# Performance work log

Measured on AMD Instinct MI355X. Metric: run time of the kernel, lower is better.

The kernel has to match this reference:

```python
import jax, jax.numpy as jnp
import numpy as np
import math

# Module constants (from __init__ defaults / chosen init_kwargs)
B = 4            # hand_batch_size
C = 8            # num_cameras
BC = B * C       # camera batch
R = 256          # resolution
NB = 64          # num_bins
BIN = 0.0136     # bin_size
FOV = 33.0       # degrees
DCS = 0.001      # camera_sensor_distance
SIGMA_BIN = 3.0  # self.sigma for soft binning


def _masks():
    fov_rad = FOV * math.pi / 180.0
    scale = math.tan(fov_rad / 2.0)
    center_scale = scale * (1.0 - 1.0 / R)
    lin = jnp.linspace(-center_scale, center_scale, R, dtype=jnp.float32)
    xg, yg = jnp.meshgrid(lin, lin, indexing='xy')
    fm = jnp.stack([xg, -yg, -jnp.ones((R, R), jnp.float32)], axis=2)
    film_mask = -fm / jnp.linalg.norm(fm, axis=2, keepdims=True)  # [R,R,3]
    cos_mask = 1.0 / jnp.sqrt(xg * xg + yg * yg + 1.0)            # [R,R]
    return film_mask, cos_mask


def setup_inputs() -> dict:
    key = jax.random.key(0)
    k1, k2 = jax.random.split(key)
    film_mask, cos_mask = _masks()
    # per-pixel interpolated vertex normals (pre-normalization, as dr.interpolate output)
    normals = jax.random.normal(k1, (BC, R, R, 3), dtype=jnp.float32)
    # per-pixel camera-space intersection points; z ~ 0.5 m so depths fall mid-histogram
    intersections = jax.random.normal(k2, (BC, R, R, 3), dtype=jnp.float32) * 0.1 \
        + jnp.array([0.0, 0.0, 0.5], dtype=jnp.float32)
    return {"normals": normals, "intersections": intersections,
            "film_mask": film_mask, "cos_mask": cos_mask}


def reference(normals, intersections, film_mask, cos_mask):
    width = 2.0 * math.tan(FOV * math.pi / 360.0)
    # cosine foreshortening w.r.t. film ray directions
    dots = jnp.clip(jnp.einsum('ijk,bijk->bij', film_mask, normals), 0.0, 1.0)
    # laser origin offset by 2 * camera_sensor_distance along +x
    laser_points = intersections - jnp.array([2.0 * DCS, 0.0, 0.0], dtype=intersections.dtype)
    laser_distances = jnp.linalg.norm(laser_points, axis=3)  # [BC,R,R]
    laser_tan = jnp.sqrt(laser_points[..., 0] ** 2 + laser_points[..., 1] ** 2) / laser_points[..., 2]
    sig = math.tan(math.radians(21.5)) / 1.4
    laser_mask = jnp.exp(-laser_tan ** 2 / (2.0 * sig * sig))
    dots = dots * laser_mask
    radiance = dots / laser_distances / laser_distances / math.pi \
        * (width * width) * (cos_mask ** 3) / float(R * R)      # [BC,R,R]
    depths = (jnp.linalg.norm(intersections, axis=3) + laser_distances) / 2.0
    d_bin = depths / BIN                                         # [BC,R,R]
    b = jnp.arange(NB, dtype=jnp.float32)                        # [NB]
    # soft bin kernel: sigmoid(s*(d-b)) - sigmoid(s*(d-b-1)), [BC,R,R,NB]
    x = d_bin[..., None] - b
    kernels = jax.nn.sigmoid(SIGMA_BIN * x) - jax.nn.sigmoid(SIGMA_BIN * (x - 1.0))
    # histogram accumulation over all pixels -> per-camera transient [BC,NB]
    transients = jnp.einsum('bijk,bij->bk', kernels, radiance)
    return transients
```

## Files before the change

### kernel.cpp

```cpp
#include <hip/hip_runtime.h>
#include <math.h>

#define NPIX    65536
#define NBINS   64
#define NBATCH  32
#define SPLIT   32
#define BLOCKT  256
#define PXPT    4
#define ITERS   (NPIX / SPLIT / (BLOCKT * PXPT))
#define WIN     12
#define HSTRIDE 68
#define NG      (BLOCKT / 2)
#define SCRATCH (4 * NBINS)
#define LDSN    (NG * HSTRIDE + SCRATCH)

#define THREE_LOG2E 4.328085122666891f

static __device__ __forceinline__ void rmw12(float* hp, const float* W) {
    float4* h4 = (float4*)hp;
    float4 a = h4[0], bb = h4[1], c = h4[2];
    a.x  += W[0];  a.y  += W[1];  a.z  += W[2];  a.w  += W[3];
    bb.x += W[4];  bb.y += W[5];  bb.z += W[6];  bb.w += W[7];
    c.x  += W[8];  c.y  += W[9];  c.z  += W[10]; c.w  += W[11];
    h4[0] = a; h4[1] = bb; h4[2] = c;
}

__global__ __launch_bounds__(BLOCKT, 4) void spad_hist_kernel(
    const float* __restrict__ normals,
    const float* __restrict__ inters,
    const float* __restrict__ film,
    const float* __restrict__ cosm,
    float* __restrict__ ws,
    float kconst, float lmask_c, float half_inv_bin,
    float xstep, float xneg)
{
    __shared__ float hist[LDSN];
    const int tid = threadIdx.x;
    for (int i = tid; i < LDSN; i += BLOCKT) hist[i] = 0.0f;
    __syncthreads();

    const int b = blockIdx.x & (NBATCH - 1);
    const int chunk = blockIdx.x / NBATCH;
    const int pix0 = chunk * (NPIX / SPLIT);
    const int gbase = (tid >> 1) * HSTRIDE;
    const int odd = tid & 1;

    const float E3P[13] = {
        1.0f, 20.085536923187668f, 403.4287934927351f, 8103.083927575384f,
        162754.79141900392f, 3269017.372472111f, 65659969.13733051f,
        1318815734.4832146f, 26489122129.843472f, 532048240601.79865f,
        10686474581524.462f, 214643579785916.06f, 4311231547115195.0f };

    #pragma unroll
    for (int it = 0; it < ITERS; ++it) {
        const int pp = pix0 + (it * BLOCKT + tid) * PXPT;
        const float4* n4 = (const float4*)(normals + ((size_t)b * NPIX + pp) * 3);
        const float4* i4 = (const float4*)(inters  + ((size_t)b * NPIX + pp) * 3);
        float4 n0 = n4[0], n1 = n4[1], n2 = n4[2];
        float4 i0 = i4[0], i1 = i4[1], i2 = i4[2];

        float NX[4] = {n0.x, n0.w, n1.z, n2.y}, NY[4] = {n0.y, n1.x, n1.w, n2.z},
              NZ[4] = {n0.z, n1.y, n2.x, n2.w};
        float IX[4] = {i0.x, i0.w, i1.z, i2.y}, IY[4] = {i0.y, i1.x, i1.w, i2.z},
              IZ[4] = {i0.z, i1.y, i2.x, i2.w};

        const float yv = fmaf((float)(pp >> 8), xstep, xneg);
        const float xb = fmaf((float)(pp & 255), xstep, xneg);
        const float y2p1 = fmaf(yv, yv, 1.0f);

        #pragma unroll
        for (int p = 0; p < 4; ++p) {
            const float xv = fmaf((float)p, xstep, xb);
            const float inorm = __builtin_amdgcn_rsqf(fmaf(xv, xv, y2p1));
            float dtr = fmaf(yv, NY[p], NZ[p]);
            dtr = fmaf(-xv, NX[p], dtr);
            float dt = fminf(fmaxf(dtr * inorm, 0.0f), 1.0f);
            const float cm3 = inorm * inorm * inorm;

            float lx = IX[p] - 0.002f;
            float lxy2 = lx * lx + IY[p] * IY[p];
            float l2 = lxy2 + IZ[p] * IZ[p];
            float ldst = __builtin_amdgcn_sqrtf(l2);
            float lm = __builtin_amdgcn_exp2f(
                lmask_c * lxy2 * __builtin_amdgcn_rcpf(IZ[p] * IZ[p]));
            float r = dt * lm * kconst * cm3 * __builtin_amdgcn_rcpf(l2);
            float di = __builtin_amdgcn_sqrtf(
                IX[p] * IX[p] + IY[p] * IY[p] + IZ[p] * IZ[p]);
            float d = (di + ldst) * half_inv_bin;

            int j0 = (int)floorf(d);
            j0 = j0 < 4 ? 4 : (j0 > 56 ? 56 : j0);
            int k0 = (j0 - 4) & ~3;
            float e0 = __builtin_amdgcn_exp2f(((float)k0 - d) * THREE_LOG2E);
            float S[WIN + 1];
            #pragma unroll
            for (int m = 0; m < WIN + 1; ++m)
                S[m] = __builtin_amdgcn_rcpf(fmaf(e0, E3P[m], 1.0f));
            float W[WIN];
            #pragma unroll
            for (int m = 0; m < WIN; ++m)
                W[m] = r * (S[m] - S[m + 1]);

            float* hp = &hist[gbase + k0];
            if (!odd) rmw12(hp, W);
            asm volatile("" ::: "memory");
            if (odd)  rmw12(hp, W);
            asm volatile("" ::: "memory");
        }
    }
    __syncthreads();

    {
        const int bin = tid & 63, s = tid >> 6;
        float sum = 0.0f;
        #pragma unroll
        for (int g = 0; g < NG / 4; ++g)
            sum += hist[(s * (NG / 4) + g) * HSTRIDE + bin];
        hist[NG * HSTRIDE + s * NBINS + bin] = sum;
    }
    __syncthreads();
    if (tid < NBINS) {
        const float* pa = &hist[NG * HSTRIDE];
        ws[(size_t)blockIdx.x * NBINS + tid] =
            pa[tid] + pa[NBINS + tid] + pa[2 * NBINS + tid] + pa[3 * NBINS + tid];
    }
}

__global__ __launch_bounds__(256) void spad_reduce_kernel(
    const float* __restrict__ ws, float* __restrict__ out)
{
    const int o = blockIdx.x * 256 + threadIdx.x;
    const int b = o >> 6;
    const int k = o & 63;
    float s = 0.0f;
    #pragma unroll
    for (int c = 0; c < SPLIT; ++c)
        s += ws[((size_t)(c * NBATCH + b)) * NBINS + k];
    out[o] = s;
}

extern "C" void kernel_launch(void* const* d_in, const int* in_sizes, int n_in,
                              void* d_out, int out_size, void* d_ws, size_t ws_size,
                              hipStream_t stream) {
    const float* normals = (const float*)d_in[0];
    const float* inters  = (const float*)d_in[1];
    const float* film    = (const float*)d_in[2];
    const float* cosm    = (const float*)d_in[3];
    float* out = (float*)d_out;
    float* ws  = (float*)d_ws;

    const double fov_rad = 33.0 * M_PI / 180.0;
    const double width = 2.0 * tan(fov_rad / 2.0);
    const double kconst_d = width * width / M_PI / 65536.0;
    const double sig = tan(21.5 * M_PI / 180.0) / 1.4;
    const double log2e = 1.4426950408889634;
    const double lmask_c_d = -log2e / (2.0 * sig * sig);
    const double half_inv_bin_d = 0.5 / 0.0136;
    const double scale = tan(fov_rad / 2.0);
    const double c_d = scale * (255.0 / 256.0);
    const float  xstep = (float)(2.0 * c_d / 255.0);
    const float  xneg  = (float)(-c_d);

    spad_hist_kernel<<<NBATCH * SPLIT, BLOCKT, 0, stream>>>(
        normals, inters, film, cosm, ws,
        (float)kconst_d, (float)lmask_c_d, (float)half_inv_bin_d,
        xstep, xneg);

    spad_reduce_kernel<<<(NBATCH * NBINS) / 256, 256, 0, stream>>>(ws, out);
}
```

Measured before the change: 93.20 us.

## Replace LDS histogram scatter with per-thread register accumulators via masked FMAs

Each thread now keeps a private 64-bin accumulator in registers. The 12-bin window is added through predicated FMAs across all 16 bin groups, using a one-hot mask on the group index, instead of read-modify-write into LDS sub-histograms. A staged LDS reduction at the end combines the per-thread histograms. This removes LDS scatter traffic and the serialized odd/even RMW, but costs about 3x64 FMAs per pixel instead of 12 adds and raises register pressure, so occupancy is lowered to 3 waves.

After: 97.19 us. 1.04x slower.

```diff
diff --git a/kernel.cpp b/kernel.cpp
--- a/kernel.cpp
+++ b/kernel.cpp
@@ -9,23 +9,11 @@
 #define PXPT    4
 #define ITERS   (NPIX / SPLIT / (BLOCKT * PXPT))
 #define WIN     12
-#define HSTRIDE 68
-#define NG      (BLOCKT / 2)
-#define SCRATCH (4 * NBINS)
-#define LDSN    (NG * HSTRIDE + SCRATCH)
+#define NGRP    16
 
 #define THREE_LOG2E 4.328085122666891f
 
-static __device__ __forceinline__ void rmw12(float* hp, const float* W) {
-    float4* h4 = (float4*)hp;
-    float4 a = h4[0], bb = h4[1], c = h4[2];
-    a.x  += W[0];  a.y  += W[1];  a.z  += W[2];  a.w  += W[3];
-    bb.x += W[4];  bb.y += W[5];  bb.z += W[6];  bb.w += W[7];
-    c.x  += W[8];  c.y  += W[9];  c.z  += W[10]; c.w  += W[11];
-    h4[0] = a; h4[1] = bb; h4[2] = c;
-}
-
-__global__ __launch_bounds__(BLOCKT, 4) void spad_hist_kernel(
+__global__ __launch_bounds__(BLOCKT, 3) void spad_hist_kernel(
     const float* __restrict__ normals,
     const float* __restrict__ inters,
     const float* __restrict__ film,
@@ -34,22 +22,22 @@
     float kconst, float lmask_c, float half_inv_bin,
     float xstep, float xneg)
 {
-    __shared__ float hist[LDSN];
+    __shared__ float red[BLOCKT * 17];
     const int tid = threadIdx.x;
-    for (int i = tid; i < LDSN; i += BLOCKT) hist[i] = 0.0f;
-    __syncthreads();
 
     const int b = blockIdx.x & (NBATCH - 1);
     const int chunk = blockIdx.x / NBATCH;
     const int pix0 = chunk * (NPIX / SPLIT);
-    const int gbase = (tid >> 1) * HSTRIDE;
-    const int odd = tid & 1;
 
     const float E3P[13] = {
         1.0f, 20.085536923187668f, 403.4287934927351f, 8103.083927575384f,
         162754.79141900392f, 3269017.372472111f, 65659969.13733051f,
         1318815734.4832146f, 26489122129.843472f, 532048240601.79865f,
         10686474581524.462f, 214643579785916.06f, 4311231547115195.0f };
+
+    float acc[NBINS];
+    #pragma unroll
+    for (int k = 0; k < NBINS; ++k) acc[k] = 0.0f;
 
     #pragma unroll
     for (int it = 0; it < ITERS; ++it) {
@@ -91,6 +79,7 @@
             int j0 = (int)floorf(d);
             j0 = j0 < 4 ? 4 : (j0 > 56 ? 56 : j0);
             int k0 = (j0 - 4) & ~3;
+            const int g0 = k0 >> 2;
             float e0 = __builtin_amdgcn_exp2f(((float)k0 - d) * THREE_LOG2E);
             float S[WIN + 1];
             #pragma unroll
@@ -98,31 +87,46 @@
                 S[m] = __builtin_amdgcn_rcpf(fmaf(e0, E3P[m], 1.0f));
             float W[WIN];
             #pragma unroll
-            for (int m = 0; m < WIN; ++m)
-                W[m] = r * (S[m] - S[m + 1]);
+            for (int m = 0; m < WIN; ++m) W[m] = S[m] - S[m + 1];
 
-            float* hp = &hist[gbase + k0];
-            if (!odd) rmw12(hp, W);
-            asm volatile("" ::: "memory");
-            if (odd)  rmw12(hp, W);
-            asm volatile("" ::: "memory");
+            float mr[14];
+            #pragma unroll
+            for (int c = 0; c < 14; ++c)
+                mr[c] = (g0 == c) ? r : 0.0f;
+
+            #pragma unroll
+            for (int g = 0; g < NGRP; ++g) {
+                #pragma unroll
+                for (int c = 0; c < 4; ++c) {
+                    float a = acc[4 * g + c];
+                    if (g <= 13)              a = fmaf(mr[g],     W[c],     a);
+                    if (g >= 1 && g <= 14)    a = fmaf(mr[g - 1], W[4 + c], a);
+                    if (g >= 2)               a = fmaf(mr[g - 2], W[8 + c], a);
+                    acc[4 * g + c] = a;
+                }
+            }
         }
     }
-    __syncthreads();
 
-    {
-        const int bin = tid & 63, s = tid >> 6;
-        float sum = 0.0f;
+    #pragma unroll
+    for (int c = 0; c < NBINS / 16; ++c) {
+        __syncthreads();
         #pragma unroll
-        for (int g = 0; g < NG / 4; ++g)
-            sum += hist[(s * (NG / 4) + g) * HSTRIDE + bin];
-        hist[NG * HSTRIDE + s * NBINS + bin] = sum;
-    }
-    __syncthreads();
-    if (tid < NBINS) {
-        const float* pa = &hist[NG * HSTRIDE];
-        ws[(size_t)blockIdx.x * NBINS + tid] =
-            pa[tid] + pa[NBINS + tid] + pa[2 * NBINS + tid] + pa[3 * NBINS + tid];
+        for (int j = 0; j < 16; ++j) red[tid * 17 + j] = acc[c * 16 + j];
+        __syncthreads();
+        const int g = tid >> 4, j = tid & 15;
+        float s = 0.0f;
+        #pragma unroll
+        for (int i = 0; i < 16; ++i) s += red[(g * 16 + i) * 17 + j];
+        __syncthreads();
+        red[tid] = s;
+        __syncthreads();
+        if (tid < 16) {
+            float rr = 0.0f;
+            #pragma unroll
+            for (int gg = 0; gg < 16; ++gg) rr += red[gg * 16 + tid];
+            ws[(size_t)blockIdx.x * NBINS + c * 16 + tid] = rr;
+        }
     }
 }
 
```
